# Optimization experiments

Hardware: AMD Instinct MI355X
Metric: run time of the kernel (lower is better)

The kernel has to match this reference:

```python
import jax, jax.numpy as jnp
import numpy as np

# ---- geometry / discretization constants (match init_kwargs) ----
IMG_H, IMG_W = 512, 512
N_VIEWS = 180
N_DET = 512
DET_SPACING = 2.0
VOXEL_SPACING = 1.0
SID = 600.0          # source-to-isocenter distance
IDD = 500.0          # isocenter-to-detector distance
N_SAMPLES = 512      # ray-marching samples per ray (Joseph-style)


def _bilinear(img, px, py):
    """Bilinear sample of 2D image at pixel coords (px=cols, py=rows); 0 outside."""
    H, W = img.shape
    ix0 = jnp.floor(px)
    iy0 = jnp.floor(py)
    fx = px - ix0
    fy = py - iy0
    ix0 = ix0.astype(jnp.int32)
    iy0 = iy0.astype(jnp.int32)
    ix1 = ix0 + 1
    iy1 = iy0 + 1
    flat = img.reshape(-1)

    def gather(iy, ix):
        valid = (ix >= 0) & (ix < W) & (iy >= 0) & (iy < H)
        idx = jnp.clip(iy, 0, H - 1) * W + jnp.clip(ix, 0, W - 1)
        return jnp.where(valid, jnp.take(flat, idx), 0.0)

    return (gather(iy0, ix0) * (1.0 - fx) * (1.0 - fy)
            + gather(iy0, ix1) * fx * (1.0 - fy)
            + gather(iy1, ix0) * (1.0 - fx) * fy
            + gather(iy1, ix1) * fx * fy)


def fan_project(img, src_pos, det_center, det_u_vec):
    """Fan-beam forward projection: line integrals src -> each detector bin.
    img: [H,W]; src_pos/det_center/det_u_vec: [V,2]. Returns sinogram [V,n_det]."""
    H, W = img.shape
    # detector bin offsets along the detector tangent, centered
    u = (jnp.arange(N_DET, dtype=img.dtype) - (N_DET - 1) / 2.0) * DET_SPACING  # [D]
    det_pts = det_center[:, None, :] + u[None, :, None] * det_u_vec[:, None, :]  # [V,D,2]
    src = src_pos[:, None, :]                                                    # [V,1,2]
    d = det_pts - src                                                            # [V,D,2]
    seg_len = jnp.sqrt(d[..., 0] ** 2 + d[..., 1] ** 2)                          # [V,D]
    # midpoint samples t in (0,1) along each ray
    t = (jnp.arange(N_SAMPLES, dtype=img.dtype) + 0.5) / N_SAMPLES               # [S]
    pts_x = src[..., 0][:, :, None] + t[None, None, :] * d[..., 0][:, :, None]   # [V,D,S]
    pts_y = src[..., 1][:, :, None] + t[None, None, :] * d[..., 1][:, :, None]   # [V,D,S]
    # world -> pixel coords (image centered at origin)
    px = pts_x / VOXEL_SPACING + (W - 1) / 2.0
    py = pts_y / VOXEL_SPACING + (H - 1) / 2.0
    vals = _bilinear(img, px, py)                                                # [V,D,S]
    return vals.sum(axis=-1) * (seg_len / N_SAMPLES)                             # [V,D]


def setup_inputs() -> dict:
    key = jax.random.key(0)
    k1, k2 = jax.random.split(key)
    x = jax.random.normal(k1, (IMG_H, IMG_W), dtype=jnp.float32)
    reco = jax.random.normal(k2, (IMG_H, IMG_W), dtype=jnp.float32) * 0.01
    ang = np.linspace(0.0, 2.0 * np.pi, N_VIEWS, endpoint=False).astype(np.float32)
    cos_a, sin_a = np.cos(ang), np.sin(ang)
    src_pos = jnp.asarray(np.stack([SID * cos_a, SID * sin_a], axis=-1))
    det_center = jnp.asarray(np.stack([-IDD * cos_a, -IDD * sin_a], axis=-1))
    det_u_vec = jnp.asarray(np.stack([-sin_a, cos_a], axis=-1))
    return {"x": x, "reco": reco, "src_pos": src_pos,
            "det_center": det_center, "det_u_vec": det_u_vec}


def reference(x, reco, src_pos, det_center, det_u_vec):
    updated = x + reco
    sino = fan_project(updated, src_pos, det_center, det_u_vec)
    return sino, jax.nn.relu(updated)
```

## Files before the change

kernel.cpp:

```cpp
#include <hip/hip_runtime.h>
#include <hip/hip_bf16.h>
#include <hip/hip_fp16.h>

#define IMG_H 512
#define IMG_W 512
#define N_VIEWS 180
#define N_DET 512
#define N_SAMPLES 512

#define N_RAYS (N_VIEWS * N_DET)
#define IMG_N (IMG_H * IMG_W)

#define QPAD 8
#define QDIM (IMG_W + 1 + 2 * QPAD)
#define Q_N (QDIM * QDIM)
#define Q_BYTES ((size_t)Q_N * sizeof(uint2))
#define RAYINFO_BYTES ((size_t)N_RAYS * 32)

#define K_CHUNKS 4

__global__ __launch_bounds__(256) void pack_q_relu_kernel(
        const float* __restrict__ x, const float* __restrict__ r,
        uint2* __restrict__ Q, float* __restrict__ relu_out) {
    int i = blockIdx.x * blockDim.x + threadIdx.x;
    if (i >= Q_N) return;
    int row = i / QDIM;
    int col = i - row * QDIM;
    int iy0 = row - QPAD, ix0 = col - QPAD;
    const bool y0v = (unsigned)iy0 < (unsigned)IMG_H;
    const bool y1v = (unsigned)(iy0 + 1) < (unsigned)IMG_H;
    const bool x0v = (unsigned)ix0 < (unsigned)IMG_W;
    const bool x1v = (unsigned)(ix0 + 1) < (unsigned)IMG_W;
    float v00 = 0.f, v01 = 0.f, v10 = 0.f, v11 = 0.f;
    if (y0v) {
        int base = iy0 * IMG_W;
        if (x0v) v00 = x[base + ix0] + r[base + ix0];
        if (x1v) v01 = x[base + ix0 + 1] + r[base + ix0 + 1];
    }
    if (y1v) {
        int base = (iy0 + 1) * IMG_W;
        if (x0v) v10 = x[base + ix0] + r[base + ix0];
        if (x1v) v11 = x[base + ix0 + 1] + r[base + ix0 + 1];
    }
    __half2 lo = __floats2half2_rn(v00, v01);
    __half2 hi = __floats2half2_rn(v10, v11);
    Q[i] = make_uint2(*reinterpret_cast<unsigned*>(&lo),
                      *reinterpret_cast<unsigned*>(&hi));
    if (y0v && x0v) relu_out[iy0 * IMG_W + ix0] = fmaxf(v00, 0.f);
}

__global__ __launch_bounds__(256) void ray_setup_kernel(
        const float* __restrict__ src_pos,
        const float* __restrict__ det_center,
        const float* __restrict__ det_u,
        float4* __restrict__ RA, float4* __restrict__ RB,
        float* __restrict__ sino) {
    const int rid = blockIdx.x * blockDim.x + threadIdx.x;
    const int v   = rid >> 9;
    const int det = rid & 511;

    const float sx = src_pos[2 * v];
    const float sy = src_pos[2 * v + 1];
    const float u  = ((float)det - 255.5f) * 2.0f;
    const float ex = det_center[2 * v]     + u * det_u[2 * v];
    const float ey = det_center[2 * v + 1] + u * det_u[2 * v + 1];

    const float dx = ex - sx;
    const float dy = ey - sy;
    const float segscl = sqrtf(dx * dx + dy * dy) * (1.0f / (float)N_SAMPLES);

    const float lo = -256.5f, hi = 256.5f;
    float t0 = 0.f, t1 = 1.f;
    if (fabsf(dx) > 1e-12f) {
        float ta = (lo - sx) / dx, tb = (hi - sx) / dx;
        t0 = fmaxf(t0, fminf(ta, tb));
        t1 = fminf(t1, fmaxf(ta, tb));
    } else if (sx <= lo || sx >= hi) {
        t1 = -1.f;
    }
    if (fabsf(dy) > 1e-12f) {
        float ta = (lo - sy) / dy, tb = (hi - sy) / dy;
        t0 = fmaxf(t0, fminf(ta, tb));
        t1 = fminf(t1, fmaxf(ta, tb));
    } else if (sy <= lo || sy >= hi) {
        t1 = -1.f;
    }
    int s0 = 0, len = 0;
    if (t1 >= t0) {
        s0 = max(0, (int)floorf(t0 * (float)N_SAMPLES - 0.5f) - 1);
        int s1 = min(N_SAMPLES - 1, (int)ceilf(t1 * (float)N_SAMPLES - 0.5f) + 1);
        len = s1 - s0 + 1;
        if (len < 0) len = 0;
    }
    RA[rid] = make_float4(dx, dy, sx + 255.5f + (float)QPAD,
                                  sy + 255.5f + (float)QPAD);
    RB[rid] = make_float4(segscl, (float)s0, (float)len, 0.f);
    sino[rid] = 0.f;
}

__device__ __forceinline__ float sample_h(const uint2* __restrict__ Q,
                                          float t, float dx, float dy,
                                          float bx, float by, float acc) {
    const float px = fmaf(t, dx, bx);
    const float py = fmaf(t, dy, by);
    const float ixf = truncf(px);
    const float iyf = truncf(py);
    const float fx = px - ixf;
    const float fy = py - iyf;
    const int lin = (int)iyf * QDIM + (int)ixf;

    const uint2 qw = Q[lin];
    const float2 fa = __half22float2(*reinterpret_cast<const __half2*>(&qw.x));
    const float2 fb = __half22float2(*reinterpret_cast<const __half2*>(&qw.y));

    const float gx = 1.f - fx;
    const float h0 = fmaf(fx, fa.y, gx * fa.x);
    const float h1 = fmaf(fx, fb.y, gx * fb.x);
    acc = fmaf(1.f - fy, h0, acc);
    acc = fmaf(fy, h1, acc);
    return acc;
}

__global__ __launch_bounds__(256) void fanproj_tile_kernel(
        const uint2* __restrict__ Q,
        const float4* __restrict__ RA, const float4* __restrict__ RB,
        float* __restrict__ sino) {
    const int tix  = threadIdx.x;
    const int lane = tix & 63;
    const int dsub = lane & 15;
    const int soff = lane >> 4;
    const int rid  = blockIdx.x * 64 + ((tix >> 6) << 4) + dsub;
    const int chunk = blockIdx.y;

    const float4 a = RA[rid];
    const float4 b = RB[rid];
    const float dx = a.x, dy = a.y, bx = a.z, by = a.w;
    const int s0  = (int)b.y;
    const int len = (int)b.z;
    const int c0 = s0 + ((len * chunk) >> 2);
    const int c1 = s0 + ((len * (chunk + 1)) >> 2) - 1;

    int s = c0 + soff;
    float t = ((float)s + 0.5f) * (1.0f / (float)N_SAMPLES);
    float acc0 = 0.f, acc1 = 0.f;
    for (; s + 4 <= c1; s += 8) {
        acc0 = sample_h(Q, t,               dx, dy, bx, by, acc0);
        acc1 = sample_h(Q, t + 0.0078125f,  dx, dy, bx, by, acc1);
        t += 0.015625f;
    }
    if (s <= c1) acc0 = sample_h(Q, t, dx, dy, bx, by, acc0);

    float acc = acc0 + acc1;
    acc += __shfl_xor(acc, 16);
    acc += __shfl_xor(acc, 32);
    if (soff == 0) {
        const float res = acc * b.x;
        if (res != 0.f) atomicAdd(&sino[rid], res);
    }
}

__global__ __launch_bounds__(256) void add_kernel(const float4* __restrict__ x,
                                                  const float4* __restrict__ r,
                                                  float4* __restrict__ upd) {
    int i = blockIdx.x * blockDim.x + threadIdx.x;
    float4 a = x[i];
    float4 b = r[i];
    upd[i] = make_float4(a.x + b.x, a.y + b.y, a.z + b.z, a.w + b.w);
}
__global__ __launch_bounds__(256) void relu_kernel(const float4* __restrict__ upd,
                                                   float4* __restrict__ out) {
    int i = blockIdx.x * blockDim.x + threadIdx.x;
    float4 c = upd[i];
    out[i] = make_float4(fmaxf(c.x, 0.f), fmaxf(c.y, 0.f),
                         fmaxf(c.z, 0.f), fmaxf(c.w, 0.f));
}

__device__ __forceinline__ float sample_plain(const float* __restrict__ img,
                                              int s, float dx, float dy,
                                              float bx, float by, float acc) {
    const float t  = fmaf((float)s, 1.f / (float)N_SAMPLES,
                          0.5f / (float)N_SAMPLES);
    const float px = fmaf(t, dx, bx);
    const float py = fmaf(t, dy, by);
    const float ix0f = floorf(px);
    const float iy0f = floorf(py);
    const float fx = px - ix0f;
    const float fy = py - iy0f;
    const int ix0 = (int)ix0f;
    const int iy0 = (int)iy0f;
    const float gx = ((unsigned)ix0       < (unsigned)IMG_W) ? (1.f - fx) : 0.f;
    const float hx = ((unsigned)(ix0 + 1) < (unsigned)IMG_W) ? fx         : 0.f;
    const float gy = ((unsigned)iy0       < (unsigned)IMG_H) ? (1.f - fy) : 0.f;
    const float hy = ((unsigned)(iy0 + 1) < (unsigned)IMG_H) ? fy         : 0.f;
    const unsigned cx0 = (unsigned)min(max(ix0, 0), IMG_W - 1);
    const unsigned cx1 = (unsigned)min(max(ix0 + 1, 0), IMG_W - 1);
    const unsigned r0  = (unsigned)min(max(iy0, 0), IMG_H - 1) << 9;
    const unsigned r1  = (unsigned)min(max(iy0 + 1, 0), IMG_H - 1) << 9;
    const float v00 = img[r0 + cx0];
    const float v01 = img[r0 + cx1];
    const float v10 = img[r1 + cx0];
    const float v11 = img[r1 + cx1];
    acc = fmaf(v00, gx * gy, acc);
    acc = fmaf(v01, hx * gy, acc);
    acc = fmaf(v10, gx * hy, acc);
    acc = fmaf(v11, hx * hy, acc);
    return acc;
}

__global__ __launch_bounds__(256) void fanproj_plain_kernel(
        const float* __restrict__ img,
        const float* __restrict__ src_pos,
        const float* __restrict__ det_center,
        const float* __restrict__ det_u,
        float* __restrict__ sino) {
    const int wid  = (blockIdx.x * blockDim.x + threadIdx.x) >> 6;
    const int lane = threadIdx.x & 63;
    if (wid >= N_RAYS) return;
    const int v   = wid >> 9;
    const int det = wid & 511;
    const float sx = src_pos[2 * v];
    const float sy = src_pos[2 * v + 1];
    const float u  = ((float)det - 255.5f) * 2.0f;
    const float ex = det_center[2 * v]     + u * det_u[2 * v];
    const float ey = det_center[2 * v + 1] + u * det_u[2 * v + 1];
    const float dx = ex - sx;
    const float dy = ey - sy;
    const float seg = sqrtf(dx * dx + dy * dy);
    const float bx = sx + 255.5f;
    const float by = sy + 255.5f;
    const float lo = -256.5f, hi = 256.5f;
    float t0 = 0.f, t1 = 1.f;
    if (fabsf(dx) > 1e-12f) {
        float ta = (lo - sx) / dx, tb = (hi - sx) / dx;
        t0 = fmaxf(t0, fminf(ta, tb));
        t1 = fminf(t1, fmaxf(ta, tb));
    } else if (sx <= lo || sx >= hi) {
        t1 = -1.f;
    }
    if (fabsf(dy) > 1e-12f) {
        float ta = (lo - sy) / dy, tb = (hi - sy) / dy;
        t0 = fmaxf(t0, fminf(ta, tb));
        t1 = fminf(t1, fmaxf(ta, tb));
    } else if (sy <= lo || sy >= hi) {
        t1 = -1.f;
    }
    int s0 = 0, s1 = -1;
    if (t1 >= t0) {
        s0 = max(0, (int)floorf(t0 * (float)N_SAMPLES - 0.5f) - 1);
        s1 = min(N_SAMPLES - 1, (int)ceilf(t1 * (float)N_SAMPLES - 0.5f) + 1);
    }
    float acc0 = 0.f, acc1 = 0.f;
    int s = s0 + lane;
    for (; s + 64 <= s1; s += 128) {
        acc0 = sample_plain(img, s,      dx, dy, bx, by, acc0);
        acc1 = sample_plain(img, s + 64, dx, dy, bx, by, acc1);
    }
    if (s <= s1) acc0 = sample_plain(img, s, dx, dy, bx, by, acc0);
    float acc = acc0 + acc1;
    #pragma unroll
    for (int off = 32; off >= 1; off >>= 1) acc += __shfl_xor(acc, off);
    if (lane == 0) sino[wid] = acc * seg * (1.0f / (float)N_SAMPLES);
}

extern "C" void kernel_launch(void* const* d_in, const int* in_sizes, int n_in,
                              void* d_out, int out_size, void* d_ws, size_t ws_size,
                              hipStream_t stream) {
    const float* x          = (const float*)d_in[0];
    const float* reco       = (const float*)d_in[1];
    const float* src_pos    = (const float*)d_in[2];
    const float* det_center = (const float*)d_in[3];
    const float* det_u      = (const float*)d_in[4];

    float* out  = (float*)d_out;
    float* sino = out;
    float* relu = out + N_RAYS;

    const int n4 = IMG_N / 4;

    if (ws_size >= Q_BYTES + RAYINFO_BYTES) {
        uint2*  Q  = (uint2*)d_ws;
        float4* RA = (float4*)((char*)d_ws + ((Q_BYTES + 255) & ~(size_t)255));
        float4* RB = RA + N_RAYS;
        pack_q_relu_kernel<<<(Q_N + 255) / 256, 256, 0, stream>>>(
            x, reco, Q, relu);
        ray_setup_kernel<<<N_RAYS / 256, 256, 0, stream>>>(
            src_pos, det_center, det_u, RA, RB, sino);
        fanproj_tile_kernel<<<dim3(N_RAYS / 64, K_CHUNKS), 256, 0, stream>>>(
            Q, RA, RB, sino);
    } else {
        float* upd = relu;
        add_kernel<<<n4 / 256, 256, 0, stream>>>(
            (const float4*)x, (const float4*)reco, (float4*)upd);
        fanproj_plain_kernel<<<N_RAYS / 4, 256, 0, stream>>>(
            upd, src_pos, det_center, det_u, sino);
        relu_kernel<<<n4 / 256, 256, 0, stream>>>(
            (const float4*)upd, (float4*)relu);
    }
}
```

Before: 44.26 us.

## Halve the fp16 quad texture to vertical pairs and merge the prep kernels

Result: faster. 36.70 us, median of 2 (-17.1%).

```diff
diff --git a/kernel.cpp b/kernel.cpp
--- a/kernel.cpp
+++ b/kernel.cpp
@@ -13,49 +13,50 @@
 
 #define QPAD 8
 #define QDIM (IMG_W + 1 + 2 * QPAD)
-#define Q_N (QDIM * QDIM)
-#define Q_BYTES ((size_t)Q_N * sizeof(uint2))
+#define R_N (QDIM * QDIM)
+#define R_BYTES ((size_t)R_N * 4)
+#define R_BYTES_AL ((R_BYTES + 255) & ~(size_t)255)
 #define RAYINFO_BYTES ((size_t)N_RAYS * 32)
 
 #define K_CHUNKS 4
-
-__global__ __launch_bounds__(256) void pack_q_relu_kernel(
+#define PACK_BLOCKS ((R_N + 255) / 256)
+#define SETUP_BLOCKS (N_RAYS / 256)
+
+__global__ __launch_bounds__(256) void prep_kernel(
         const float* __restrict__ x, const float* __restrict__ r,
-        uint2* __restrict__ Q, float* __restrict__ relu_out) {
-    int i = blockIdx.x * blockDim.x + threadIdx.x;
-    if (i >= Q_N) return;
-    int row = i / QDIM;
-    int col = i - row * QDIM;
-    int iy0 = row - QPAD, ix0 = col - QPAD;
-    const bool y0v = (unsigned)iy0 < (unsigned)IMG_H;
-    const bool y1v = (unsigned)(iy0 + 1) < (unsigned)IMG_H;
-    const bool x0v = (unsigned)ix0 < (unsigned)IMG_W;
-    const bool x1v = (unsigned)(ix0 + 1) < (unsigned)IMG_W;
-    float v00 = 0.f, v01 = 0.f, v10 = 0.f, v11 = 0.f;
-    if (y0v) {
-        int base = iy0 * IMG_W;
-        if (x0v) v00 = x[base + ix0] + r[base + ix0];
-        if (x1v) v01 = x[base + ix0 + 1] + r[base + ix0 + 1];
-    }
-    if (y1v) {
-        int base = (iy0 + 1) * IMG_W;
-        if (x0v) v10 = x[base + ix0] + r[base + ix0];
-        if (x1v) v11 = x[base + ix0 + 1] + r[base + ix0 + 1];
-    }
-    __half2 lo = __floats2half2_rn(v00, v01);
-    __half2 hi = __floats2half2_rn(v10, v11);
-    Q[i] = make_uint2(*reinterpret_cast<unsigned*>(&lo),
-                      *reinterpret_cast<unsigned*>(&hi));
-    if (y0v && x0v) relu_out[iy0 * IMG_W + ix0] = fmaxf(v00, 0.f);
-}
-
-__global__ __launch_bounds__(256) void ray_setup_kernel(
+        unsigned* __restrict__ R, float* __restrict__ relu_out,
         const float* __restrict__ src_pos,
         const float* __restrict__ det_center,
         const float* __restrict__ det_u,
         float4* __restrict__ RA, float4* __restrict__ RB,
         float* __restrict__ sino) {
-    const int rid = blockIdx.x * blockDim.x + threadIdx.x;
+    const int b = blockIdx.x;
+    if (b < PACK_BLOCKS) {
+        int i = b * 256 + threadIdx.x;
+        if (i >= R_N) return;
+        int row = i / QDIM;
+        int col = i - row * QDIM;
+        int yy = row - QPAD;
+        int xx = col - QPAD;
+        float v0 = 0.f, v1 = 0.f;
+        if ((unsigned)xx < (unsigned)IMG_W) {
+            if ((unsigned)yy < (unsigned)IMG_H) {
+                int idx = yy * IMG_W + xx;
+                v0 = x[idx] + r[idx];
+            }
+            if ((unsigned)(yy + 1) < (unsigned)IMG_H) {
+                int idx = (yy + 1) * IMG_W + xx;
+                v1 = x[idx] + r[idx];
+            }
+        }
+        __half2 h = __floats2half2_rn(v0, v1);
+        R[i] = *reinterpret_cast<unsigned*>(&h);
+        if ((unsigned)xx < (unsigned)IMG_W && (unsigned)yy < (unsigned)IMG_H)
+            relu_out[yy * IMG_W + xx] = fmaxf(v0, 0.f);
+        return;
+    }
+
+    const int rid = (b - PACK_BLOCKS) * 256 + threadIdx.x;
     const int v   = rid >> 9;
     const int det = rid & 511;
 
@@ -98,7 +99,7 @@
     sino[rid] = 0.f;
 }
 
-__device__ __forceinline__ float sample_h(const uint2* __restrict__ Q,
+__device__ __forceinline__ float sample_h(const unsigned* __restrict__ R,
                                           float t, float dx, float dy,
                                           float bx, float by, float acc) {
     const float px = fmaf(t, dx, bx);
@@ -109,20 +110,21 @@
     const float fy = py - iyf;
     const int lin = (int)iyf * QDIM + (int)ixf;
 
-    const uint2 qw = Q[lin];
+    uint2 qw;
+    __builtin_memcpy(&qw, R + lin, 8);
     const float2 fa = __half22float2(*reinterpret_cast<const __half2*>(&qw.x));
     const float2 fb = __half22float2(*reinterpret_cast<const __half2*>(&qw.y));
 
     const float gx = 1.f - fx;
-    const float h0 = fmaf(fx, fa.y, gx * fa.x);
-    const float h1 = fmaf(fx, fb.y, gx * fb.x);
+    const float h0 = fmaf(fx, fb.x, gx * fa.x);
+    const float h1 = fmaf(fx, fb.y, gx * fa.y);
     acc = fmaf(1.f - fy, h0, acc);
     acc = fmaf(fy, h1, acc);
     return acc;
 }
 
 __global__ __launch_bounds__(256) void fanproj_tile_kernel(
-        const uint2* __restrict__ Q,
+        const unsigned* __restrict__ R,
         const float4* __restrict__ RA, const float4* __restrict__ RB,
         float* __restrict__ sino) {
     const int tix  = threadIdx.x;
@@ -144,11 +146,11 @@
     float t = ((float)s + 0.5f) * (1.0f / (float)N_SAMPLES);
     float acc0 = 0.f, acc1 = 0.f;
     for (; s + 4 <= c1; s += 8) {
-        acc0 = sample_h(Q, t,               dx, dy, bx, by, acc0);
-        acc1 = sample_h(Q, t + 0.0078125f,  dx, dy, bx, by, acc1);
+        acc0 = sample_h(R, t,               dx, dy, bx, by, acc0);
+        acc1 = sample_h(R, t + 0.0078125f,  dx, dy, bx, by, acc1);
         t += 0.015625f;
     }
-    if (s <= c1) acc0 = sample_h(Q, t, dx, dy, bx, by, acc0);
+    if (s <= c1) acc0 = sample_h(R, t, dx, dy, bx, by, acc0);
 
     float acc = acc0 + acc1;
     acc += __shfl_xor(acc, 16);
@@ -277,16 +279,14 @@
 
     const int n4 = IMG_N / 4;
 
-    if (ws_size >= Q_BYTES + RAYINFO_BYTES) {
-        uint2*  Q  = (uint2*)d_ws;
-        float4* RA = (float4*)((char*)d_ws + ((Q_BYTES + 255) & ~(size_t)255));
-        float4* RB = RA + N_RAYS;
-        pack_q_relu_kernel<<<(Q_N + 255) / 256, 256, 0, stream>>>(
-            x, reco, Q, relu);
-        ray_setup_kernel<<<N_RAYS / 256, 256, 0, stream>>>(
-            src_pos, det_center, det_u, RA, RB, sino);
+    if (ws_size >= R_BYTES_AL + RAYINFO_BYTES) {
+        unsigned* R  = (unsigned*)d_ws;
+        float4*   RA = (float4*)((char*)d_ws + R_BYTES_AL);
+        float4*   RB = RA + N_RAYS;
+        prep_kernel<<<PACK_BLOCKS + SETUP_BLOCKS, 256, 0, stream>>>(
+            x, reco, R, relu, src_pos, det_center, det_u, RA, RB, sino);
         fanproj_tile_kernel<<<dim3(N_RAYS / 64, K_CHUNKS), 256, 0, stream>>>(
-            Q, RA, RB, sino);
+            R, RA, RB, sino);
     } else {
         float* upd = relu;
         add_kernel<<<n4 / 256, 256, 0, stream>>>(
```
